# Performance work log

Measured on AMD Instinct MI355X. Metric: run time of the kernel, lower is better.

## Reference

```python
import jax, jax.numpy as jnp
import numpy as np

B, S, D = 8, 1024, 256
H, DH = 8, 32  # num_heads, head_dim; H*DH == D


def setup_inputs() -> dict:
    key = jax.random.key(0)
    ks = jax.random.split(key, 10)
    s = 0.02
    return {
        "q": jax.random.normal(ks[0], (B, S, D), jnp.float32),
        "k": jax.random.normal(ks[1], (B, S, D), jnp.float32),
        "v": jax.random.normal(ks[2], (B, S, D), jnp.float32),
        "mask": jnp.zeros((B, 1, 1, S), jnp.float32),  # additive mask
        "bias": jax.random.normal(ks[3], (1, H, S, S), jnp.float32),  # pair bias
        "Wq": jax.random.normal(ks[4], (H * DH, D), jnp.float32) * s,
        "Wk": jax.random.normal(ks[5], (H * DH, D), jnp.float32) * s,
        "Wv": jax.random.normal(ks[6], (H * DH, D), jnp.float32) * s,
        "Wg": jnp.zeros((H * DH, D), jnp.float32),   # gating init: zeros weight
        "bg": jnp.ones((H * DH,), jnp.float32),      # gating init: ones bias
        "Wo": jax.random.normal(ks[7], (D, H * DH), jnp.float32) * s,
    }


def reference(q, k, v, mask, bias, Wq, Wk, Wv, Wg, bg, Wo):
    norm = DH ** -0.5
    g = jnp.einsum('bsd,ed->bse', q, Wg) + bg            # [B,S,H*DH]
    qh = (jnp.einsum('bsd,ed->bse', q, Wq) * norm).reshape(B, S, H, DH)
    kh = jnp.einsum('bsd,ed->bse', k, Wk).reshape(B, S, H, DH)
    vh = jnp.einsum('bsd,ed->bse', v, Wv).reshape(B, S, H, DH)
    # scores [B,H,Q,K] with additive mask and pair bias (unicore softmax_dropout)
    attn = jnp.einsum('bqhd,bkhd->bhqk', qh, kh) + mask + bias
    attn = jax.nn.softmax(attn, axis=-1)
    o = jnp.einsum('bhqk,bkhd->bqhd', attn, vh).reshape(B, S, H * DH)
    o = jax.nn.sigmoid(g) * o                            # gating
    return jnp.einsum('bse,de->bsd', o, Wo)              # output proj, NO bias in fwd
```

## Files before the change

kernel.cpp:

```cpp
#include <hip/hip_runtime.h>


typedef __attribute__((ext_vector_type(4))) float f32x4;
typedef __attribute__((ext_vector_type(8))) unsigned short u16x8;
typedef __attribute__((ext_vector_type(4))) unsigned short u16x4;
typedef __attribute__((ext_vector_type(8))) __bf16 bf16x8;
typedef __attribute__((ext_vector_type(4))) __bf16 bf16x4;

#define BB 8
#define SS 1024
#define DD 256
#define HH 8
#define DHD 32

__device__ __forceinline__ float b2f(unsigned short s) {
  unsigned u = ((unsigned)s) << 16;
  return __builtin_bit_cast(float, u);
}
__device__ __forceinline__ f32x4 mfma16(u16x8 a, u16x8 b, f32x4 c) {
  return __builtin_amdgcn_mfma_f32_16x16x32_bf16(
      __builtin_bit_cast(bf16x8, a), __builtin_bit_cast(bf16x8, b), c, 0, 0, 0);
}

__device__ __forceinline__ void gload_lds16(const unsigned short* gsrc,
                                            unsigned short* ldst) {
#if __has_builtin(__builtin_amdgcn_global_load_lds)
  __builtin_amdgcn_global_load_lds(
      (const __attribute__((address_space(1))) unsigned int*)gsrc,
      (__attribute__((address_space(3))) unsigned int*)ldst, 16, 0, 0);
#else
  *(u16x8*)ldst = *(const u16x8*)gsrc;
#endif
}

__global__ __launch_bounds__(256) void proj_kernel(
    const float* __restrict__ q, const float* __restrict__ k,
    const float* __restrict__ v,
    const float* __restrict__ Wq, const float* __restrict__ Wg,
    const float* __restrict__ Wk, const float* __restrict__ Wv,
    const float* __restrict__ bg,
    unsigned short* __restrict__ qh, unsigned short* __restrict__ kh,
    unsigned short* __restrict__ vhT, unsigned short* __restrict__ sig) {
  const int slot = blockIdx.z;
  const float* A = (slot <= 1) ? q : (slot == 2 ? k : v);
  const float* W = (slot == 0) ? Wq : (slot == 1 ? Wg : (slot == 2 ? Wk : Wv));
  const int row0 = blockIdx.x * 64, col0 = blockIdx.y * 64;
  const int tid = threadIdx.x;
  const int w = tid >> 6, lane = tid & 63, g = lane >> 4, c = lane & 15;
  const int sr = tid >> 2, sc = tid & 3;

  __shared__ alignas(16) unsigned short As[64 * 32];
  __shared__ alignas(16) unsigned short Ws[64 * 32];

  const f32x4 zero = {0.f, 0.f, 0.f, 0.f};
  f32x4 acc[4] = {zero, zero, zero, zero};

  for (int kk = 0; kk < 8; ++kk) {
    __syncthreads();
    {
      const float* ap = A + (size_t)(row0 + sr) * DD + kk * 32 + sc * 8;
      f32x4 f0 = *(const f32x4*)ap;
      f32x4 f1 = *(const f32x4*)(ap + 4);
      bf16x8 a8;
#pragma unroll
      for (int j = 0; j < 4; ++j) { a8[j] = (__bf16)f0[j]; a8[j + 4] = (__bf16)f1[j]; }
      ((u16x8*)As)[sr * 4 + (sc ^ ((sr >> 1) & 3))] = __builtin_bit_cast(u16x8, a8);

      const float* wp = W + (size_t)(col0 + sr) * DD + kk * 32 + sc * 8;
      f32x4 w0 = *(const f32x4*)wp;
      f32x4 w1 = *(const f32x4*)(wp + 4);
      bf16x8 w8;
#pragma unroll
      for (int j = 0; j < 4; ++j) { w8[j] = (__bf16)w0[j]; w8[j + 4] = (__bf16)w1[j]; }
      ((u16x8*)Ws)[sr * 4 + (sc ^ ((sr >> 1) & 3))] = __builtin_bit_cast(u16x8, w8);
    }
    __syncthreads();
    const int arow = 16 * w + c;
    u16x8 af = ((u16x8*)As)[arow * 4 + (g ^ ((arow >> 1) & 3))];
#pragma unroll
    for (int n = 0; n < 4; ++n) {
      const int brow = 16 * n + c;
      u16x8 wf = ((u16x8*)Ws)[brow * 4 + (g ^ ((brow >> 1) & 3))];
      acc[n] = mfma16(af, wf, acc[n]);
    }
  }

  if (slot == 3) {
    const int row_base = row0 + 16 * w + 4 * g;
    const int bb = row_base >> 10;
    const int s0 = row_base & 1023;
#pragma unroll
    for (int n = 0; n < 4; ++n) {
      const int col = col0 + 16 * n + c;
      bf16x4 pv;
#pragma unroll
      for (int r = 0; r < 4; ++r) pv[r] = (__bf16)acc[n][r];
      *(u16x4*)(vhT + (size_t)(bb * 256 + col) * SS + s0) =
          __builtin_bit_cast(u16x4, pv);
    }
  } else {
#pragma unroll
    for (int n = 0; n < 4; ++n) {
#pragma unroll
      for (int r = 0; r < 4; ++r) {
        const int row = row0 + 16 * w + 4 * g + r;
        const int col = col0 + 16 * n + c;
        const size_t idx = (size_t)row * DD + col;
        const float val = acc[n][r];
        if (slot == 0)
          qh[idx] = __builtin_bit_cast(unsigned short,
                        (__bf16)(val * 0.17677669529663687f));
        else if (slot == 1)
          sig[idx] = __builtin_bit_cast(unsigned short,
                         (__bf16)(1.0f / (1.0f + __expf(-(val + bg[col])))));
        else
          kh[idx] = __builtin_bit_cast(unsigned short, (__bf16)val);
      }
    }
  }
}

__global__ __launch_bounds__(256, 2) void attn_kernel(
    const unsigned short* __restrict__ qh, const unsigned short* __restrict__ kh,
    const unsigned short* __restrict__ vhT, const unsigned short* __restrict__ sig,
    const float* __restrict__ mask, const float* __restrict__ bias,
    unsigned short* __restrict__ og) {
  const int bid = blockIdx.x;
  const int widx = (bid & 7) * 128 + (bid >> 3);
  const int h = widx >> 7, b = (widx >> 4) & 7, qt = widx & 15;
  const int tid = threadIdx.x;
  const int w = tid >> 6, lane = tid & 63, g = lane >> 4, c = lane & 15;

  __shared__ alignas(16) unsigned short KsB[2][256 * 32];
  __shared__ alignas(16) unsigned short VtB[2][32 * 256];
  __shared__ alignas(16) unsigned short Ps[4][16 * 64];
  unsigned short* P = Ps[w];

  const int q0 = qt * 64 + w * 16;
  const u16x8 qf =
      *(const u16x8*)(qh + (size_t)(b * SS + q0 + c) * DD + h * DHD + g * 8);

  const f32x4 zero = {0.f, 0.f, 0.f, 0.f};
  f32x4 acc[2] = {zero, zero};
  float m_r = -1e30f, l_r = 0.f;

  const float* maskb = mask + b * SS;
  const float* biasb = bias + (size_t)(h * SS + q0 + c) * SS;

  auto stage = [&](int buf, int kv0) {
    unsigned short* Kb = KsB[buf];
    unsigned short* Vb = VtB[buf];
#pragma unroll
    for (int i = 0; i < 4; ++i) {
      const int s = i * 256 + tid;
      const int krow = s >> 2, kc = s & 3;
      const int klc = kc ^ ((krow >> 1) & 3);
      gload_lds16(kh + (size_t)(b * SS + kv0 + krow) * DD + h * DHD + klc * 8,
                  Kb + s * 8);
      const int vr = s >> 5, jp = s & 31;
      const int jl = (jp & 24) | ((jp & 7) ^ (vr & 7));
      gload_lds16(vhT + (size_t)((b * HH + h) * DHD + vr) * SS + kv0 + jl * 8,
                  Vb + s * 8);
    }
  };

  stage(0, 0);
  __syncthreads();

#pragma unroll 1
  for (int kt = 0; kt < 4; ++kt) {
    const int cur = kt & 1;
    const int kv0 = kt * 256;
    if (kt < 3) stage(cur ^ 1, kv0 + 256);

    const u16x8* Ks16 = (const u16x8*)KsB[cur];
    const u16x8* Vt16 = (const u16x8*)VtB[cur];

#pragma unroll
    for (int gr = 0; gr < 4; ++gr) {
      const int kvg = kv0 + gr * 64;
      f32x4 sv[4];
#pragma unroll
      for (int t = 0; t < 4; ++t) {
        const u16x8 kf =
            Ks16[(gr * 64 + 16 * t + c) * 4 + (g ^ ((c >> 1) & 3))];
        sv[t] = mfma16(kf, qf, zero);
      }
#pragma unroll
      for (int t = 0; t < 4; ++t) {
        const f32x4 bi = *(const f32x4*)(biasb + kvg + 16 * t + 4 * g);
        const f32x4 mk = *(const f32x4*)(maskb + kvg + 16 * t + 4 * g);
        sv[t] += bi + mk;
      }
      float pm = fmaxf(fmaxf(sv[0][0], sv[0][1]), fmaxf(sv[0][2], sv[0][3]));
#pragma unroll
      for (int t = 1; t < 4; ++t)
        pm = fmaxf(pm,
                   fmaxf(fmaxf(sv[t][0], sv[t][1]), fmaxf(sv[t][2], sv[t][3])));
      if (!__all(pm - m_r <= 8.0f)) {
        float mx = fmaxf(pm, __shfl_xor(pm, 16));
        mx = fmaxf(mx, __shfl_xor(mx, 32));
        const float mnew = fmaxf(m_r, mx);
        const float scale = __expf(m_r - mnew);
        l_r *= scale;
        acc[0] *= scale;
        acc[1] *= scale;
        m_r = mnew;
      }
      float ps = 0.f;
#pragma unroll
      for (int t = 0; t < 4; ++t)
#pragma unroll
        for (int r = 0; r < 4; ++r) {
          const float p = __expf(sv[t][r] - m_r);
          sv[t][r] = p;
          ps += p;
        }
      l_r += ps;
#pragma unroll
      for (int t = 0; t < 4; ++t) {
        bf16x4 pv;
#pragma unroll
        for (int r = 0; r < 4; ++r) pv[r] = (__bf16)sv[t][r];
        const int n = 2 * t + (g >> 1);
        *(u16x4*)(P + c * 64 + ((n ^ (c & 7)) << 3) + ((g & 1) << 2)) =
            __builtin_bit_cast(u16x4, pv);
      }
#pragma unroll
      for (int s2 = 0; s2 < 2; ++s2) {
        const u16x8 pf =
            *(const u16x8*)(P + c * 64 + (((4 * s2 + g) ^ (c & 7)) << 3));
#pragma unroll
        for (int dt = 0; dt < 2; ++dt) {
          const u16x8 vf =
              Vt16[(16 * dt + c) * 32 + gr * 8 + ((4 * s2 + g) ^ (c & 7))];
          acc[dt] = mfma16(vf, pf, acc[dt]);
        }
      }
    }
    __syncthreads();
  }

  float l = l_r + __shfl_xor(l_r, 16);
  l += __shfl_xor(l, 32);
  const float inv = 1.0f / l;
#pragma unroll
  for (int dt = 0; dt < 2; ++dt) {
    const size_t idx =
        (size_t)(b * SS + q0 + c) * DD + h * DHD + 16 * dt + 4 * g;
    const u16x4 sg = *(const u16x4*)(sig + idx);
    bf16x4 ov;
#pragma unroll
    for (int r = 0; r < 4; ++r) ov[r] = (__bf16)(acc[dt][r] * inv * b2f(sg[r]));
    *(u16x4*)(og + idx) = __builtin_bit_cast(u16x4, ov);
  }
}

__global__ __launch_bounds__(256) void outproj_kernel(
    const unsigned short* __restrict__ og, const float* __restrict__ Wo,
    float* __restrict__ out) {
  const int row0 = blockIdx.x * 64, col0 = blockIdx.y * 64;
  const int tid = threadIdx.x;
  const int w = tid >> 6, lane = tid & 63, g = lane >> 4, c = lane & 15;
  const int sr = tid >> 2, sc = tid & 3;

  __shared__ alignas(16) unsigned short As[64 * 32];
  __shared__ alignas(16) unsigned short Ws[64 * 32];

  const f32x4 zero = {0.f, 0.f, 0.f, 0.f};
  f32x4 acc[4] = {zero, zero, zero, zero};

  for (int kk = 0; kk < 8; ++kk) {
    __syncthreads();
    {
      const unsigned short* ap = og + (size_t)(row0 + sr) * DD + kk * 32 + sc * 8;
      ((u16x8*)As)[sr * 4 + (sc ^ ((sr >> 1) & 3))] = *(const u16x8*)ap;

      const float* wp = Wo + (size_t)(col0 + sr) * DD + kk * 32 + sc * 8;
      f32x4 w0 = *(const f32x4*)wp;
      f32x4 w1 = *(const f32x4*)(wp + 4);
      bf16x8 w8;
#pragma unroll
      for (int j = 0; j < 4; ++j) { w8[j] = (__bf16)w0[j]; w8[j + 4] = (__bf16)w1[j]; }
      ((u16x8*)Ws)[sr * 4 + (sc ^ ((sr >> 1) & 3))] = __builtin_bit_cast(u16x8, w8);
    }
    __syncthreads();
    const int arow = 16 * w + c;
    u16x8 af = ((u16x8*)As)[arow * 4 + (g ^ ((arow >> 1) & 3))];
#pragma unroll
    for (int n = 0; n < 4; ++n) {
      const int brow = 16 * n + c;
      u16x8 wf = ((u16x8*)Ws)[brow * 4 + (g ^ ((brow >> 1) & 3))];
      acc[n] = mfma16(af, wf, acc[n]);
    }
  }

#pragma unroll
  for (int n = 0; n < 4; ++n) {
#pragma unroll
    for (int r = 0; r < 4; ++r) {
      const int row = row0 + 16 * w + 4 * g + r;
      const int col = col0 + 16 * n + c;
      out[(size_t)row * DD + col] = acc[n][r];
    }
  }
}

extern "C" void kernel_launch(void* const* d_in, const int* in_sizes, int n_in,
                              void* d_out, int out_size, void* d_ws,
                              size_t ws_size, hipStream_t stream) {
  const float* q    = (const float*)d_in[0];
  const float* k    = (const float*)d_in[1];
  const float* v    = (const float*)d_in[2];
  const float* mask = (const float*)d_in[3];
  const float* bias = (const float*)d_in[4];
  const float* Wq   = (const float*)d_in[5];
  const float* Wk   = (const float*)d_in[6];
  const float* Wv   = (const float*)d_in[7];
  const float* Wg   = (const float*)d_in[8];
  const float* bg   = (const float*)d_in[9];
  const float* Wo   = (const float*)d_in[10];
  float* out = (float*)d_out;

  char* ws = (char*)d_ws;
  unsigned short* qh  = (unsigned short*)(ws);
  unsigned short* kh  = (unsigned short*)(ws + (4u << 20));
  unsigned short* vhT = (unsigned short*)(ws + (8u << 20));
  unsigned short* sig = (unsigned short*)(ws + (12u << 20));
  unsigned short* og  = (unsigned short*)(ws + (16u << 20));

  hipLaunchKernelGGL(proj_kernel, dim3(128, 4, 4), dim3(256), 0, stream,
                     q, k, v, Wq, Wg, Wk, Wv, bg, qh, kh, vhT, sig);
  hipLaunchKernelGGL(attn_kernel, dim3(1024), dim3(256), 0, stream,
                     qh, kh, vhT, sig, mask, bias, og);
  hipLaunchKernelGGL(outproj_kernel, dim3(128, 4), dim3(256), 0, stream,
                     og, Wo, out);
}
```

Baseline: 80.24 us.

## Halve attention KV tile, raise occupancy, split softmax into two streams

The attention kernel now stages 128-key tiles instead of 256, which halves shared memory per block, and raises the launch-bounds occupancy hint from 2 to 4 blocks per CU. Each 128-key tile is processed as two independent 64-key online-softmax streams with their own max, sum and accumulators, merged once at the end. The goal is more latency hiding from extra resident waves and two independent dependency chains that can interleave. The costs are twice as many tile iterations and barriers, plus more live registers, which could cause spills under the tighter register budget.

```diff
diff --git a/kernel.cpp b/kernel.cpp
--- a/kernel.cpp
+++ b/kernel.cpp
@@ -120,7 +120,7 @@
   }
 }
 
-__global__ __launch_bounds__(256, 2) void attn_kernel(
+__global__ __launch_bounds__(256, 4) void attn_kernel(
     const unsigned short* __restrict__ qh, const unsigned short* __restrict__ kh,
     const unsigned short* __restrict__ vhT, const unsigned short* __restrict__ sig,
     const float* __restrict__ mask, const float* __restrict__ bias,
@@ -131,8 +131,8 @@
   const int tid = threadIdx.x;
   const int w = tid >> 6, lane = tid & 63, g = lane >> 4, c = lane & 15;
 
-  __shared__ alignas(16) unsigned short KsB[2][256 * 32];
-  __shared__ alignas(16) unsigned short VtB[2][32 * 256];
+  __shared__ alignas(16) unsigned short KsB[2][128 * 32];
+  __shared__ alignas(16) unsigned short VtB[2][32 * 128];
   __shared__ alignas(16) unsigned short Ps[4][16 * 64];
   unsigned short* P = Ps[w];
 
@@ -141,8 +141,9 @@
       *(const u16x8*)(qh + (size_t)(b * SS + q0 + c) * DD + h * DHD + g * 8);
 
   const f32x4 zero = {0.f, 0.f, 0.f, 0.f};
-  f32x4 acc[2] = {zero, zero};
-  float m_r = -1e30f, l_r = 0.f;
+  f32x4 aA0 = zero, aA1 = zero, aB0 = zero, aB1 = zero;
+  float mA = -1e30f, lA = 0.f;
+  float mB = -1e30f, lB = 0.f;
 
   const float* maskb = mask + b * SS;
   const float* biasb = bias + (size_t)(h * SS + q0 + c) * SS;
@@ -151,107 +152,115 @@
     unsigned short* Kb = KsB[buf];
     unsigned short* Vb = VtB[buf];
 #pragma unroll
-    for (int i = 0; i < 4; ++i) {
+    for (int i = 0; i < 2; ++i) {
       const int s = i * 256 + tid;
       const int krow = s >> 2, kc = s & 3;
       const int klc = kc ^ ((krow >> 1) & 3);
       gload_lds16(kh + (size_t)(b * SS + kv0 + krow) * DD + h * DHD + klc * 8,
                   Kb + s * 8);
-      const int vr = s >> 5, jp = s & 31;
-      const int jl = (jp & 24) | ((jp & 7) ^ (vr & 7));
+      const int vr = s >> 4, jp = s & 15;
+      const int jl = (jp & 8) | ((jp & 7) ^ (vr & 7));
       gload_lds16(vhT + (size_t)((b * HH + h) * DHD + vr) * SS + kv0 + jl * 8,
                   Vb + s * 8);
     }
   };
 
+  auto stream64 = [&](const u16x8* Ks16, const u16x8* Vt16, int gr, int kv_abs,
+                      f32x4& a0, f32x4& a1, float& m_r, float& l_r) {
+    f32x4 sv[4];
+#pragma unroll
+    for (int t = 0; t < 4; ++t) {
+      const u16x8 kf =
+          Ks16[(gr * 64 + 16 * t + c) * 4 + (g ^ ((c >> 1) & 3))];
+      sv[t] = mfma16(kf, qf, zero);
+    }
+#pragma unroll
+    for (int t = 0; t < 4; ++t) {
+      const f32x4 bi = *(const f32x4*)(biasb + kv_abs + 16 * t + 4 * g);
+      const f32x4 mk = *(const f32x4*)(maskb + kv_abs + 16 * t + 4 * g);
+      sv[t] += bi + mk;
+    }
+    float pm = fmaxf(fmaxf(sv[0][0], sv[0][1]), fmaxf(sv[0][2], sv[0][3]));
+#pragma unroll
+    for (int t = 1; t < 4; ++t)
+      pm = fmaxf(pm,
+                 fmaxf(fmaxf(sv[t][0], sv[t][1]), fmaxf(sv[t][2], sv[t][3])));
+    if (!__all(pm - m_r <= 8.0f)) {
+      float mx = fmaxf(pm, __shfl_xor(pm, 16));
+      mx = fmaxf(mx, __shfl_xor(mx, 32));
+      const float mnew = fmaxf(m_r, mx);
+      const float scale = __expf(m_r - mnew);
+      l_r *= scale;
+      a0 *= scale;
+      a1 *= scale;
+      m_r = mnew;
+    }
+    float ps = 0.f;
+#pragma unroll
+    for (int t = 0; t < 4; ++t)
+#pragma unroll
+      for (int r = 0; r < 4; ++r) {
+        const float p = __expf(sv[t][r] - m_r);
+        sv[t][r] = p;
+        ps += p;
+      }
+    l_r += ps;
+#pragma unroll
+    for (int t = 0; t < 4; ++t) {
+      bf16x4 pv;
+#pragma unroll
+      for (int r = 0; r < 4; ++r) pv[r] = (__bf16)sv[t][r];
+      const int n = 2 * t + (g >> 1);
+      *(u16x4*)(P + c * 64 + ((n ^ (c & 7)) << 3) + ((g & 1) << 2)) =
+          __builtin_bit_cast(u16x4, pv);
+    }
+#pragma unroll
+    for (int s2 = 0; s2 < 2; ++s2) {
+      const u16x8 pf =
+          *(const u16x8*)(P + c * 64 + (((4 * s2 + g) ^ (c & 7)) << 3));
+#pragma unroll
+      for (int dt = 0; dt < 2; ++dt) {
+        const u16x8 vf =
+            Vt16[(16 * dt + c) * 16 + gr * 8 + ((4 * s2 + g) ^ (c & 7))];
+        if (dt == 0) a0 = mfma16(vf, pf, a0);
+        else         a1 = mfma16(vf, pf, a1);
+      }
+    }
+  };
+
   stage(0, 0);
   __syncthreads();
 
 #pragma unroll 1
-  for (int kt = 0; kt < 4; ++kt) {
+  for (int kt = 0; kt < 8; ++kt) {
     const int cur = kt & 1;
-    const int kv0 = kt * 256;
-    if (kt < 3) stage(cur ^ 1, kv0 + 256);
+    const int kv0 = kt * 128;
+    if (kt < 7) stage(cur ^ 1, kv0 + 128);
 
     const u16x8* Ks16 = (const u16x8*)KsB[cur];
     const u16x8* Vt16 = (const u16x8*)VtB[cur];
 
-#pragma unroll
-    for (int gr = 0; gr < 4; ++gr) {
-      const int kvg = kv0 + gr * 64;
-      f32x4 sv[4];
-#pragma unroll
-      for (int t = 0; t < 4; ++t) {
-        const u16x8 kf =
-            Ks16[(gr * 64 + 16 * t + c) * 4 + (g ^ ((c >> 1) & 3))];
-        sv[t] = mfma16(kf, qf, zero);
-      }
-#pragma unroll
-      for (int t = 0; t < 4; ++t) {
-        const f32x4 bi = *(const f32x4*)(biasb + kvg + 16 * t + 4 * g);
-        const f32x4 mk = *(const f32x4*)(maskb + kvg + 16 * t + 4 * g);
-        sv[t] += bi + mk;
-      }
-      float pm = fmaxf(fmaxf(sv[0][0], sv[0][1]), fmaxf(sv[0][2], sv[0][3]));
-#pragma unroll
-      for (int t = 1; t < 4; ++t)
-        pm = fmaxf(pm,
-                   fmaxf(fmaxf(sv[t][0], sv[t][1]), fmaxf(sv[t][2], sv[t][3])));
-      if (!__all(pm - m_r <= 8.0f)) {
-        float mx = fmaxf(pm, __shfl_xor(pm, 16));
-        mx = fmaxf(mx, __shfl_xor(mx, 32));
-        const float mnew = fmaxf(m_r, mx);
-        const float scale = __expf(m_r - mnew);
-        l_r *= scale;
-        acc[0] *= scale;
-        acc[1] *= scale;
-        m_r = mnew;
-      }
-      float ps = 0.f;
-#pragma unroll
-      for (int t = 0; t < 4; ++t)
-#pragma unroll
-        for (int r = 0; r < 4; ++r) {
-          const float p = __expf(sv[t][r] - m_r);
-          sv[t][r] = p;
-          ps += p;
-        }
-      l_r += ps;
-#pragma unroll
-      for (int t = 0; t < 4; ++t) {
-        bf16x4 pv;
-#pragma unroll
-        for (int r = 0; r < 4; ++r) pv[r] = (__bf16)sv[t][r];
-        const int n = 2 * t + (g >> 1);
-        *(u16x4*)(P + c * 64 + ((n ^ (c & 7)) << 3) + ((g & 1) << 2)) =
-            __builtin_bit_cast(u16x4, pv);
-      }
-#pragma unroll
-      for (int s2 = 0; s2 < 2; ++s2) {
-        const u16x8 pf =
-            *(const u16x8*)(P + c * 64 + (((4 * s2 + g) ^ (c & 7)) << 3));
-#pragma unroll
-        for (int dt = 0; dt < 2; ++dt) {
-          const u16x8 vf =
-              Vt16[(16 * dt + c) * 32 + gr * 8 + ((4 * s2 + g) ^ (c & 7))];
-          acc[dt] = mfma16(vf, pf, acc[dt]);
-        }
-      }
-    }
-    __syncthreads();
-  }
-
-  float l = l_r + __shfl_xor(l_r, 16);
+    stream64(Ks16, Vt16, 0, kv0,      aA0, aA1, mA, lA);
+    stream64(Ks16, Vt16, 1, kv0 + 64, aB0, aB1, mB, lB);
+
+    __syncthreads();
+  }
+
+  const float M = fmaxf(mA, mB);
+  const float eA = __expf(mA - M), eB = __expf(mB - M);
+  float lp = lA * eA + lB * eB;
+  float l = lp + __shfl_xor(lp, 16);
   l += __shfl_xor(l, 32);
   const float inv = 1.0f / l;
 #pragma unroll
   for (int dt = 0; dt < 2; ++dt) {
+    const f32x4 am = (dt == 0) ? (aA0 * eA + aB0 * eB) : (aA1 * eA + aB1 * eB);
     const size_t idx =
         (size_t)(b * SS + q0 + c) * DD + h * DHD + 16 * dt + 4 * g;
     const u16x4 sg = *(const u16x4*)(sig + idx);
     bf16x4 ov;
 #pragma unroll
-    for (int r = 0; r < 4; ++r) ov[r] = (__bf16)(acc[dt][r] * inv * b2f(sg[r]));
+    for (int r = 0; r < 4; ++r) ov[r] = (__bf16)(am[r] * inv * b2f(sg[r]));
     *(u16x4*)(og + idx) = __builtin_bit_cast(u16x4, ov);
   }
 }
```

After: 80.50 us. No clear change (+0.3%).

## Rewrite attention kernel with 32x32 MFMA, 2-wave blocks, and 64-key tiles

Applied to the files above, without the earlier changes.

The attention kernel now uses 32x32x16 bf16 MFMA, with each wave owning 32 query rows instead of 16. The P matrix stays in registers as the B operand, which removes the LDS round trip for probabilities. Blocks shrink to 128 threads and key/value tiles shrink to 64 keys across 16 iterations, using new LDS swizzles. Bias and mask loads are issued before staging, and exp is rewritten as exp2 with a fused multiply-add. This cuts LDS traffic and instruction count but adds more sync iterations and smaller blocks, which changes occupancy.

```diff
diff --git a/kernel.cpp b/kernel.cpp
--- a/kernel.cpp
+++ b/kernel.cpp
@@ -2,6 +2,7 @@
 
 
 typedef __attribute__((ext_vector_type(4))) float f32x4;
+typedef __attribute__((ext_vector_type(16))) float f32x16;
 typedef __attribute__((ext_vector_type(8))) unsigned short u16x8;
 typedef __attribute__((ext_vector_type(4))) unsigned short u16x4;
 typedef __attribute__((ext_vector_type(8))) __bf16 bf16x8;
@@ -12,6 +13,7 @@
 #define DD 256
 #define HH 8
 #define DHD 32
+#define L2E 1.4426950408889634f
 
 __device__ __forceinline__ float b2f(unsigned short s) {
   unsigned u = ((unsigned)s) << 16;
@@ -19,6 +21,10 @@
 }
 __device__ __forceinline__ f32x4 mfma16(u16x8 a, u16x8 b, f32x4 c) {
   return __builtin_amdgcn_mfma_f32_16x16x32_bf16(
+      __builtin_bit_cast(bf16x8, a), __builtin_bit_cast(bf16x8, b), c, 0, 0, 0);
+}
+__device__ __forceinline__ f32x16 mfma32(u16x8 a, u16x8 b, f32x16 c) {
+  return __builtin_amdgcn_mfma_f32_32x32x16_bf16(
       __builtin_bit_cast(bf16x8, a), __builtin_bit_cast(bf16x8, b), c, 0, 0, 0);
 }
 
@@ -120,7 +126,7 @@
   }
 }
 
-__global__ __launch_bounds__(256, 2) void attn_kernel(
+__global__ __launch_bounds__(128, 2) void attn_kernel(
     const unsigned short* __restrict__ qh, const unsigned short* __restrict__ kh,
     const unsigned short* __restrict__ vhT, const unsigned short* __restrict__ sig,
     const float* __restrict__ mask, const float* __restrict__ bias,
@@ -129,38 +135,38 @@
   const int widx = (bid & 7) * 128 + (bid >> 3);
   const int h = widx >> 7, b = (widx >> 4) & 7, qt = widx & 15;
   const int tid = threadIdx.x;
-  const int w = tid >> 6, lane = tid & 63, g = lane >> 4, c = lane & 15;
-
-  __shared__ alignas(16) unsigned short KsB[2][256 * 32];
-  __shared__ alignas(16) unsigned short VtB[2][32 * 256];
-  __shared__ alignas(16) unsigned short Ps[4][16 * 64];
-  unsigned short* P = Ps[w];
-
-  const int q0 = qt * 64 + w * 16;
-  const u16x8 qf =
-      *(const u16x8*)(qh + (size_t)(b * SS + q0 + c) * DD + h * DHD + g * 8);
-
-  const f32x4 zero = {0.f, 0.f, 0.f, 0.f};
-  f32x4 acc[2] = {zero, zero};
+  const int w = tid >> 6, lane = tid & 63;
+  const int qc = lane & 31, hi = lane >> 5;
+
+  __shared__ alignas(16) unsigned short KsB[2][64 * 32];
+  __shared__ alignas(16) unsigned short VtB[2][32 * 64];
+
+  const int qrow = qt * 64 + w * 32 + qc;
+  const unsigned short* qp = qh + (size_t)(b * SS + qrow) * DD + h * DHD;
+  const u16x8 qf0 = *(const u16x8*)(qp + 8 * hi);
+  const u16x8 qf1 = *(const u16x8*)(qp + 16 + 8 * hi);
+
+  f32x16 acc = {};
   float m_r = -1e30f, l_r = 0.f;
 
   const float* maskb = mask + b * SS;
-  const float* biasb = bias + (size_t)(h * SS + q0 + c) * SS;
+  const float* biasq = bias + ((size_t)h * SS + qrow) * SS;
 
   auto stage = [&](int buf, int kv0) {
     unsigned short* Kb = KsB[buf];
     unsigned short* Vb = VtB[buf];
 #pragma unroll
-    for (int i = 0; i < 4; ++i) {
-      const int s = i * 256 + tid;
-      const int krow = s >> 2, kc = s & 3;
-      const int klc = kc ^ ((krow >> 1) & 3);
-      gload_lds16(kh + (size_t)(b * SS + kv0 + krow) * DD + h * DHD + klc * 8,
-                  Kb + s * 8);
-      const int vr = s >> 5, jp = s & 31;
-      const int jl = (jp & 24) | ((jp & 7) ^ (vr & 7));
-      gload_lds16(vhT + (size_t)((b * HH + h) * DHD + vr) * SS + kv0 + jl * 8,
-                  Vb + s * 8);
+    for (int i = 0; i < 2; ++i) {
+      const int s = i * 128 + tid;
+      const int kr = s >> 2, pc = s & 3;
+      gload_lds16(
+          kh + (size_t)(b * SS + kv0 + kr) * DD + h * DHD + (pc ^ (kr & 3)) * 8,
+          Kb + s * 8);
+      const int vr = s >> 3, pj = s & 7;
+      const int lu = (2 * pj) ^ ((vr & 7) << 1);
+      gload_lds16(
+          vhT + (size_t)((b * HH + h) * DHD + vr) * SS + kv0 + lu * 4,
+          Vb + s * 8);
     }
   };
 
@@ -168,90 +174,103 @@
   __syncthreads();
 
 #pragma unroll 1
-  for (int kt = 0; kt < 4; ++kt) {
-    const int cur = kt & 1;
-    const int kv0 = kt * 256;
-    if (kt < 3) stage(cur ^ 1, kv0 + 256);
-
-    const u16x8* Ks16 = (const u16x8*)KsB[cur];
-    const u16x8* Vt16 = (const u16x8*)VtB[cur];
-
-#pragma unroll
-    for (int gr = 0; gr < 4; ++gr) {
-      const int kvg = kv0 + gr * 64;
-      f32x4 sv[4];
-#pragma unroll
-      for (int t = 0; t < 4; ++t) {
-        const u16x8 kf =
-            Ks16[(gr * 64 + 16 * t + c) * 4 + (g ^ ((c >> 1) & 3))];
-        sv[t] = mfma16(kf, qf, zero);
-      }
-#pragma unroll
-      for (int t = 0; t < 4; ++t) {
-        const f32x4 bi = *(const f32x4*)(biasb + kvg + 16 * t + 4 * g);
-        const f32x4 mk = *(const f32x4*)(maskb + kvg + 16 * t + 4 * g);
-        sv[t] += bi + mk;
-      }
-      float pm = fmaxf(fmaxf(sv[0][0], sv[0][1]), fmaxf(sv[0][2], sv[0][3]));
-#pragma unroll
-      for (int t = 1; t < 4; ++t)
-        pm = fmaxf(pm,
-                   fmaxf(fmaxf(sv[t][0], sv[t][1]), fmaxf(sv[t][2], sv[t][3])));
-      if (!__all(pm - m_r <= 8.0f)) {
-        float mx = fmaxf(pm, __shfl_xor(pm, 16));
-        mx = fmaxf(mx, __shfl_xor(mx, 32));
-        const float mnew = fmaxf(m_r, mx);
-        const float scale = __expf(m_r - mnew);
-        l_r *= scale;
-        acc[0] *= scale;
-        acc[1] *= scale;
-        m_r = mnew;
-      }
-      float ps = 0.f;
-#pragma unroll
-      for (int t = 0; t < 4; ++t)
-#pragma unroll
-        for (int r = 0; r < 4; ++r) {
-          const float p = __expf(sv[t][r] - m_r);
-          sv[t][r] = p;
-          ps += p;
-        }
-      l_r += ps;
-#pragma unroll
-      for (int t = 0; t < 4; ++t) {
-        bf16x4 pv;
-#pragma unroll
-        for (int r = 0; r < 4; ++r) pv[r] = (__bf16)sv[t][r];
-        const int n = 2 * t + (g >> 1);
-        *(u16x4*)(P + c * 64 + ((n ^ (c & 7)) << 3) + ((g & 1) << 2)) =
-            __builtin_bit_cast(u16x4, pv);
-      }
-#pragma unroll
-      for (int s2 = 0; s2 < 2; ++s2) {
-        const u16x8 pf =
-            *(const u16x8*)(P + c * 64 + (((4 * s2 + g) ^ (c & 7)) << 3));
-#pragma unroll
-        for (int dt = 0; dt < 2; ++dt) {
-          const u16x8 vf =
-              Vt16[(16 * dt + c) * 32 + gr * 8 + ((4 * s2 + g) ^ (c & 7))];
-          acc[dt] = mfma16(vf, pf, acc[dt]);
-        }
-      }
-    }
-    __syncthreads();
-  }
-
-  float l = l_r + __shfl_xor(l_r, 16);
-  l += __shfl_xor(l, 32);
-  const float inv = 1.0f / l;
-#pragma unroll
-  for (int dt = 0; dt < 2; ++dt) {
-    const size_t idx =
-        (size_t)(b * SS + q0 + c) * DD + h * DHD + 16 * dt + 4 * g;
+  for (int kt = 0; kt < 16; ++kt) {
+    const int cur = kt & 1, kv0 = kt * 64;
+
+    f32x4 bm[2][4];
+#pragma unroll
+    for (int t = 0; t < 2; ++t)
+#pragma unroll
+      for (int rq = 0; rq < 4; ++rq) {
+        const int off = kv0 + 32 * t + 8 * rq + 4 * hi;
+        const f32x4 bi = *(const f32x4*)(biasq + off);
+        const f32x4 mk = *(const f32x4*)(maskb + off);
+        bm[t][rq] = bi + mk;
+      }
+
+    if (kt < 15) stage(cur ^ 1, kv0 + 64);
+
+    const unsigned short* Kb = KsB[cur];
+    const unsigned short* Vb = VtB[cur];
+
+    f32x16 sv[2];
+#pragma unroll
+    for (int t = 0; t < 2; ++t) {
+      const int kr = 32 * t + qc;
+      const u16x8 ka = ((const u16x8*)Kb)[kr * 4 + (hi ^ (kr & 3))];
+      const u16x8 kb2 = ((const u16x8*)Kb)[kr * 4 + ((2 + hi) ^ (kr & 3))];
+      f32x16 z = {};
+      z = mfma32(ka, qf0, z);
+      sv[t] = mfma32(kb2, qf1, z);
+    }
+
+#pragma unroll
+    for (int t = 0; t < 2; ++t)
+#pragma unroll
+      for (int rq = 0; rq < 4; ++rq)
+#pragma unroll
+        for (int j = 0; j < 4; ++j) sv[t][4 * rq + j] += bm[t][rq][j];
+
+    float pm = sv[0][0];
+#pragma unroll
+    for (int j = 1; j < 16; ++j) pm = fmaxf(pm, sv[0][j]);
+#pragma unroll
+    for (int j = 0; j < 16; ++j) pm = fmaxf(pm, sv[1][j]);
+    if (!__all(pm - m_r <= 8.0f)) {
+      const float mx = fmaxf(pm, __shfl_xor(pm, 32));
+      const float mnew = fmaxf(m_r, mx);
+      const float sc = exp2f((m_r - mnew) * L2E);
+      l_r *= sc;
+      acc = acc * sc;
+      m_r = mnew;
+    }
+
+    const float nm = -m_r * L2E;
+    float ps = 0.f;
+#pragma unroll
+    for (int t = 0; t < 2; ++t)
+#pragma unroll
+      for (int j = 0; j < 16; ++j) {
+        const float p = exp2f(__builtin_fmaf(sv[t][j], L2E, nm));
+        sv[t][j] = p;
+        ps += p;
+      }
+    l_r += ps;
+
+#pragma unroll
+    for (int t = 0; t < 2; ++t) {
+      bf16x8 p0, p1;
+#pragma unroll
+      for (int j = 0; j < 8; ++j) {
+        p0[j] = (__bf16)sv[t][j];
+        p1[j] = (__bf16)sv[t][8 + j];
+      }
+#pragma unroll
+      for (int ks = 0; ks < 2; ++ks) {
+        const int u1 = 8 * t + 4 * ks + hi;
+        const int sw = (qc & 7) << 1;
+        const u16x4 va = *(const u16x4*)(Vb + qc * 64 + (u1 ^ sw) * 4);
+        const u16x4 vb2 = *(const u16x4*)(Vb + qc * 64 + ((u1 | 2) ^ sw) * 4);
+        const u16x8 vf = {va[0], va[1], va[2], va[3],
+                          vb2[0], vb2[1], vb2[2], vb2[3]};
+        acc = mfma32(vf, __builtin_bit_cast(u16x8, ks == 0 ? p0 : p1), acc);
+      }
+    }
+
+    __syncthreads();
+  }
+
+  const float lp = l_r + __shfl_xor(l_r, 32);
+  const float inv = 1.0f / lp;
+#pragma unroll
+  for (int rq = 0; rq < 4; ++rq) {
+    const int dh0 = 8 * rq + 4 * hi;
+    const size_t idx = (size_t)(b * SS + qrow) * DD + h * DHD + dh0;
     const u16x4 sg = *(const u16x4*)(sig + idx);
     bf16x4 ov;
 #pragma unroll
-    for (int r = 0; r < 4; ++r) ov[r] = (__bf16)(acc[dt][r] * inv * b2f(sg[r]));
+    for (int j = 0; j < 4; ++j)
+      ov[j] = (__bf16)(acc[4 * rq + j] * inv * b2f(sg[j]));
     *(u16x4*)(og + idx) = __builtin_bit_cast(u16x4, ov);
   }
 }
@@ -331,7 +350,7 @@
 
   hipLaunchKernelGGL(proj_kernel, dim3(128, 4, 4), dim3(256), 0, stream,
                      q, k, v, Wq, Wg, Wk, Wv, bg, qh, kh, vhT, sig);
-  hipLaunchKernelGGL(attn_kernel, dim3(1024), dim3(256), 0, stream,
+  hipLaunchKernelGGL(attn_kernel, dim3(1024), dim3(128), 0, stream,
                      qh, kh, vhT, sig, mask, bias, og);
   hipLaunchKernelGGL(outproj_kernel, dim3(128, 4), dim3(256), 0, stream,
                      og, Wo, out);
```

Measured after the change: 87.70 us. 1.09x slower.
